# Kernel optimization log

Measured on AMD Instinct MI355X. Metric: run time of the kernel, lower is better.

## Reference

```python
import jax, jax.numpy as jnp
import numpy as np

H = 4       # N_head
C = 32      # c_hidden
CZ = 128    # c_z
N = 256
B = 1
EPS = 1e-5


def setup_inputs() -> dict:
    key = jax.random.key(0)
    ks = jax.random.split(key, 8)
    hc = H * C
    return {
        "z": jax.random.normal(ks[0], (B, N, N, CZ), dtype=jnp.float32),
        "ln_scale": jnp.ones((CZ,), dtype=jnp.float32),
        "ln_bias": jnp.zeros((CZ,), dtype=jnp.float32),
        "Wq": jax.random.normal(ks[1], (CZ, hc), dtype=jnp.float32) * 0.02,
        "Wk": jax.random.normal(ks[2], (CZ, hc), dtype=jnp.float32) * 0.02,
        "Wv": jax.random.normal(ks[3], (CZ, hc), dtype=jnp.float32) * 0.02,
        "Wb": jax.random.normal(ks[4], (CZ, H), dtype=jnp.float32) * 0.02,
        "Wg": jax.random.normal(ks[5], (CZ, hc), dtype=jnp.float32) * 0.02,
        "Wo": jax.random.normal(ks[6], (hc, CZ), dtype=jnp.float32) * 0.02,
    }


def reference(z, ln_scale, ln_bias, Wq, Wk, Wv, Wb, Wg, Wo):
    b, n = z.shape[0], z.shape[1]
    # LayerNorm over c_z
    mu = jnp.mean(z, axis=-1, keepdims=True)
    var = jnp.mean(jnp.square(z - mu), axis=-1, keepdims=True)
    zn = (z - mu) * jax.lax.rsqrt(var + EPS) * ln_scale + ln_bias
    # projections -> [B, N, N, H, C]
    q = (zn @ Wq).reshape(b, n, n, H, C)
    k = (zn @ Wk).reshape(b, n, n, H, C)
    v = (zn @ Wv).reshape(b, n, n, H, C)
    bias = zn @ Wb                                  # [B, N, N, H]
    g = jax.nn.sigmoid(zn @ Wg).reshape(b, n, n, H, C)
    # attention around starting node i: query at (i,j), keys/values at (i,k)
    scores = jnp.einsum('bijhd,bikhd->bijkh', q, k) * (1.0 / C ** 0.5)
    scores = scores + bias[:, None, :, :, :]        # bias[b, j, k, h]
    a = jax.nn.softmax(scores, axis=-2)             # softmax over k
    o = jnp.einsum('bijkh,bikhd->bijhd', a, v)      # [B, N, N, H, C]
    o = (g * o).reshape(b, n, n, H * C)
    return o @ Wo
```

## Files before the change

kernel.cpp:

```cpp
#include <hip/hip_runtime.h>
#include <math.h>

#define NN 256
#define CZ 128
#define NH 4
#define CH 32
#define HC 128
#define NPIX (NN*NN)
#define L2E   1.4426950408889634f
#define SCALE2 (0.17677669529663687f * 1.4426950408889634f)

typedef __attribute__((ext_vector_type(8))) short bf16x8;
typedef __attribute__((ext_vector_type(4))) float fx4;
typedef __attribute__((ext_vector_type(4))) unsigned u32x4;

__device__ __forceinline__ unsigned pack_hl(float x) {
    unsigned b  = __builtin_bit_cast(unsigned, x);
    unsigned hb = b & 0xFFFF0000u;
    float r = x - __builtin_bit_cast(float, hb);
    return hb | (__builtin_bit_cast(unsigned, r) >> 16);
}
__device__ __forceinline__ void load_split8(const float* p, bf16x8& h, bf16x8& l) {
    float4 x0 = *(const float4*)p;
    float4 x1 = *(const float4*)(p + 4);
    float xs[8] = {x0.x, x0.y, x0.z, x0.w, x1.x, x1.y, x1.z, x1.w};
    #pragma unroll
    for (int j = 0; j < 8; ++j) {
        unsigned b  = __builtin_bit_cast(unsigned, xs[j]);
        unsigned hb = b & 0xFFFF0000u;
        float r = xs[j] - __builtin_bit_cast(float, hb);
        h[j] = (short)(hb >> 16);
        l[j] = (short)(__builtin_bit_cast(unsigned, r) >> 16);
    }
}
__device__ __forceinline__ void deint8(const unsigned* p, bf16x8& h, bf16x8& l) {
    u32x4 e0 = *(const u32x4*)p;
    u32x4 e1 = *(const u32x4*)(p + 4);
    unsigned es[8] = {e0[0], e0[1], e0[2], e0[3], e1[0], e1[1], e1[2], e1[3]};
    unsigned hw[4], lw[4];
    #pragma unroll
    for (int j = 0; j < 4; ++j) {
        unsigned a = es[2 * j], b = es[2 * j + 1];
        hw[j] = (a >> 16) | (b & 0xFFFF0000u);
        lw[j] = (a & 0x0000FFFFu) | (b << 16);
    }
    h = __builtin_bit_cast(bf16x8, u32x4{hw[0], hw[1], hw[2], hw[3]});
    l = __builtin_bit_cast(bf16x8, u32x4{lw[0], lw[1], lw[2], lw[3]});
}

__device__ __forceinline__ void qtrans(unsigned &x, unsigned &y) {
#if __has_builtin(__builtin_amdgcn_permlane32_swap) && __has_builtin(__builtin_amdgcn_permlane16_swap)
    {
        auto r = __builtin_amdgcn_permlane32_swap(x, y, false, false);
        x = r[0]; y = r[1];
    }
    {
        auto r = __builtin_amdgcn_permlane16_swap(x, y, false, false);
        x = r[0]; y = r[1];
    }
#else
    asm("v_permlane32_swap_b32 %0, %1\n\t"
        "v_permlane16_swap_b32 %0, %1" : "+v"(x), "+v"(y));
#endif
}

__global__ __launch_bounds__(256) void pack_w_kernel(
    const float* __restrict__ Wq, const float* __restrict__ Wk,
    const float* __restrict__ Wv, const float* __restrict__ Wg,
    const float* __restrict__ Wo, bf16x8* __restrict__ pk)
{
    int id  = blockIdx.x * 256 + threadIdx.x;
    int mid = id >> 11;
    int e   = id & 2047;
    const float* W = (mid == 0) ? Wq : (mid == 1) ? Wk : (mid == 2) ? Wv : (mid == 3) ? Wg : Wo;
    int quad = e & 3, n = (e >> 2) & 127, ks = e >> 9;
    int k0 = ks * 32 + quad * 8;
    bf16x8 h, l;
    #pragma unroll
    for (int j = 0; j < 8; ++j) {
        float x = W[(size_t)(k0 + j) * 128 + n];
        unsigned b  = __builtin_bit_cast(unsigned, x);
        unsigned hb = b & 0xFFFF0000u;
        float r = x - __builtin_bit_cast(float, hb);
        h[j] = (short)(hb >> 16);
        l[j] = (short)(__builtin_bit_cast(unsigned, r) >> 16);
    }
    pk[(size_t)mid * 4096 + e]        = h;
    pk[(size_t)mid * 4096 + 2048 + e] = l;
}

__global__ __launch_bounds__(256) void ln_proj_kernel(
    const float* __restrict__ z, const float* __restrict__ ls, const float* __restrict__ lb,
    const float* __restrict__ Wb, const bf16x8* __restrict__ pk,
    unsigned* __restrict__ q_pk, unsigned* __restrict__ k_pk, unsigned* __restrict__ v_pk,
    float* __restrict__ g_ws, float* __restrict__ bias_n)
{
    __shared__ float zsh[32][132];
    __shared__ float rsum[256], rsq[256];
    __shared__ float pmu[32], prs[32];

    const int t  = threadIdx.x;
    const int p0 = blockIdx.x * 32;
    const int i  = p0 >> 8;
    const int j0 = p0 & 255;

    const float4* z4 = (const float4*)(z + (size_t)p0 * CZ);
    #pragma unroll
    for (int r = 0; r < 4; ++r) {
        int idx4 = t + 256 * r;
        int p = idx4 >> 5, pos = idx4 & 31;
        *(float4*)&zsh[p][pos * 4] = z4[idx4];
    }
    __syncthreads();

    {
        int p = t >> 3, sg = t & 7;
        float s = 0.f, q = 0.f;
        #pragma unroll
        for (int u = 0; u < 16; ++u) { float x = zsh[p][sg * 16 + u]; s += x; q += x * x; }
        rsum[t] = s; rsq[t] = q;
    }
    __syncthreads();
    if (t < 32) {
        float s = 0.f, q = 0.f;
        #pragma unroll
        for (int g = 0; g < 8; ++g) { s += rsum[t * 8 + g]; q += rsq[t * 8 + g]; }
        float mu  = s * (1.0f / 128.0f);
        float var = q * (1.0f / 128.0f) - mu * mu;
        float a   = var + 1e-5f;
        float r   = rsqrtf(a);
        r = r * (1.5f - 0.5f * a * r * r);
        pmu[t] = mu; prs[t] = r;
    }
    __syncthreads();

    #pragma unroll
    for (int r4 = 0; r4 < 4; ++r4) {
        int idx4 = t + 256 * r4;
        int p = idx4 >> 5, pos = idx4 & 31;
        float4 v  = *(float4*)&zsh[p][pos * 4];
        float4 s4 = ((const float4*)ls)[pos];
        float4 b4 = ((const float4*)lb)[pos];
        float mu = pmu[p], rs = prs[p];
        v.x = (v.x - mu) * rs * s4.x + b4.x;
        v.y = (v.y - mu) * rs * s4.y + b4.y;
        v.z = (v.z - mu) * rs * s4.z + b4.z;
        v.w = (v.w - mu) * rs * s4.w + b4.w;
        *(float4*)&zsh[p][pos * 4] = v;
    }
    __syncthreads();

    const int wv = t >> 6, lane = t & 63;
    const int lrow = lane & 15, quad = lane >> 4;
    const bf16x8* ph = pk + (size_t)wv * 4096;
    const bf16x8* pl = ph + 2048;

    fx4 acc[2][8];
    #pragma unroll
    for (int mr = 0; mr < 2; ++mr)
        #pragma unroll
        for (int nc = 0; nc < 8; ++nc)
            acc[mr][nc] = fx4{0.f, 0.f, 0.f, 0.f};

    #pragma unroll
    for (int ks = 0; ks < 4; ++ks) {
        bf16x8 ah[2], al[2];
        #pragma unroll
        for (int mr = 0; mr < 2; ++mr)
            load_split8(&zsh[mr * 16 + lrow][ks * 32 + quad * 8], ah[mr], al[mr]);
        #pragma unroll
        for (int nc = 0; nc < 8; ++nc) {
            int bi = (ks * 128 + nc * 16 + lrow) * 4 + quad;
            bf16x8 bh = ph[bi], bl = pl[bi];
            #pragma unroll
            for (int mr = 0; mr < 2; ++mr) {
                acc[mr][nc] = __builtin_amdgcn_mfma_f32_16x16x32_bf16(ah[mr], bl, acc[mr][nc], 0, 0, 0);
                acc[mr][nc] = __builtin_amdgcn_mfma_f32_16x16x32_bf16(al[mr], bh, acc[mr][nc], 0, 0, 0);
                acc[mr][nc] = __builtin_amdgcn_mfma_f32_16x16x32_bf16(ah[mr], bh, acc[mr][nc], 0, 0, 0);
            }
        }
    }

    #pragma unroll
    for (int mr = 0; mr < 2; ++mr) {
        #pragma unroll
        for (int nc = 0; nc < 8; ++nc) {
            int cg = nc * 16 + lrow;
            int h = cg >> 5, cc = cg & 31;
            int jl = mr * 16 + quad * 4;
            fx4 a = acc[mr][nc];
            if (wv == 0) {
                unsigned* qp = q_pk + ((size_t)(i * NH + h) * NN + j0 + jl) * CH + cc;
                #pragma unroll
                for (int r = 0; r < 4; ++r) qp[r * CH] = pack_hl(a[r]);
            } else if (wv == 1) {
                unsigned* kp = k_pk + ((size_t)(i * NH + h) * NN + j0 + jl) * CH + cc;
                #pragma unroll
                for (int r = 0; r < 4; ++r) kp[r * CH] = pack_hl(a[r]);
            } else if (wv == 2) {
                u32x4 e = {pack_hl(a[0]), pack_hl(a[1]), pack_hl(a[2]), pack_hl(a[3])};
                *(u32x4*)(v_pk + ((size_t)(i * NH + h) * CH + cc) * NN + j0 + jl) = e;
            } else {
                float* gp = g_ws + (size_t)(p0 + jl) * HC + cg;
                #pragma unroll
                for (int r = 0; r < 4; ++r) gp[r * HC] = 1.0f / (1.0f + __expf(-a[r]));
            }
        }
    }

    if (t < 128) {
        int hh = t >> 5, p = t & 31;
        float b = 0.f;
        for (int d = 0; d < 128; ++d) b = fmaf(zsh[p][d], Wb[d * 4 + hh], b);
        bias_n[(size_t)hh * NPIX + (size_t)i * NN + j0 + p] = b * L2E;
    }
}

__global__ __launch_bounds__(256) void attn_kernel(
    const unsigned* __restrict__ q_pk, const unsigned* __restrict__ k_pk,
    const unsigned* __restrict__ v_pk, const float* __restrict__ g_ws,
    const float* __restrict__ bias_n, float* __restrict__ go_ws)
{
    const int t = threadIdx.x;
    const int wv = t >> 6, lane = t & 63;
    const int lrow = lane & 15, quad = lane >> 4;
    const int h = blockIdx.x & 3, i = blockIdx.x >> 2;
    const int qb = wv * 64;

    const unsigned* qs = q_pk + (size_t)(i * NH + h) * NN * CH;
    const unsigned* ks = k_pk + (size_t)(i * NH + h) * NN * CH;
    const unsigned* vs = v_pk + (size_t)(i * NH + h) * CH * NN;
    const float*    bs = bias_n + (size_t)h * NPIX;

    bf16x8 qh[4], ql[4];
    #pragma unroll
    for (int nt = 0; nt < 4; ++nt)
        deint8(qs + (size_t)(qb + nt * 16 + lrow) * CH + quad * 8, qh[nt], ql[nt]);

    fx4 oacc[2][4];
    #pragma unroll
    for (int ct = 0; ct < 2; ++ct)
        #pragma unroll
        for (int nt = 0; nt < 4; ++nt)
            oacc[ct][nt] = fx4{0.f, 0.f, 0.f, 0.f};
    float lsum[4] = {0.f, 0.f, 0.f, 0.f};

    for (int kb = 0; kb < NN; kb += 32) {
        bf16x8 kh[2], kl_[2];
        #pragma unroll
        for (int mt = 0; mt < 2; ++mt)
            deint8(ks + (size_t)(kb + mt * 16 + lrow) * CH + quad * 8, kh[mt], kl_[mt]);
        bf16x8 vh[2], vl[2];
        #pragma unroll
        for (int ct = 0; ct < 2; ++ct)
            deint8(vs + (size_t)(ct * 16 + lrow) * NN + kb + quad * 8, vh[ct], vl[ct]);

        #pragma unroll
        for (int nt = 0; nt < 4; ++nt) {
            unsigned w0h[2], w1h[2], w0l[2], w1l[2];
            #pragma unroll
            for (int mt = 0; mt < 2; ++mt) {
                float4 bv = *(const float4*)(bs + (size_t)(qb + nt * 16 + lrow) * NN
                                                + kb + mt * 16 + quad * 4);

                fx4 sv = fx4{0.f, 0.f, 0.f, 0.f};
                __builtin_amdgcn_s_setprio(1);
                sv = __builtin_amdgcn_mfma_f32_16x16x32_bf16(kh[mt], ql[nt], sv, 0, 0, 0);
                sv = __builtin_amdgcn_mfma_f32_16x16x32_bf16(kl_[mt], qh[nt], sv, 0, 0, 0);
                sv = __builtin_amdgcn_mfma_f32_16x16x32_bf16(kh[mt], qh[nt], sv, 0, 0, 0);
                __builtin_amdgcn_s_setprio(0);

                float e0 = exp2f(fmaf(sv[0], SCALE2, bv.x));
                float e1 = exp2f(fmaf(sv[1], SCALE2, bv.y));
                float e2 = exp2f(fmaf(sv[2], SCALE2, bv.z));
                float e3 = exp2f(fmaf(sv[3], SCALE2, bv.w));
                lsum[nt] += (e0 + e1) + (e2 + e3);

                unsigned b0 = __builtin_bit_cast(unsigned, e0);
                unsigned b1 = __builtin_bit_cast(unsigned, e1);
                unsigned b2 = __builtin_bit_cast(unsigned, e2);
                unsigned b3 = __builtin_bit_cast(unsigned, e3);
                unsigned h01 = (b0 >> 16) | (b1 & 0xFFFF0000u);
                unsigned h23 = (b2 >> 16) | (b3 & 0xFFFF0000u);
                float r0 = e0 - __builtin_bit_cast(float, b0 & 0xFFFF0000u);
                float r1 = e1 - __builtin_bit_cast(float, b1 & 0xFFFF0000u);
                float r2 = e2 - __builtin_bit_cast(float, b2 & 0xFFFF0000u);
                float r3 = e3 - __builtin_bit_cast(float, b3 & 0xFFFF0000u);
                unsigned l01 = (__builtin_bit_cast(unsigned, r0) >> 16)
                             | (__builtin_bit_cast(unsigned, r1) & 0xFFFF0000u);
                unsigned l23 = (__builtin_bit_cast(unsigned, r2) >> 16)
                             | (__builtin_bit_cast(unsigned, r3) & 0xFFFF0000u);
                w0h[mt] = h01; w1h[mt] = h23;
                w0l[mt] = l01; w1l[mt] = l23;
            }

            qtrans(w0h[0], w0h[1]);
            qtrans(w1h[0], w1h[1]);
            qtrans(w0l[0], w0l[1]);
            qtrans(w1l[0], w1l[1]);
            bf16x8 pbh = __builtin_bit_cast(bf16x8, u32x4{w0h[0], w1h[0], w0h[1], w1h[1]});
            bf16x8 pbl = __builtin_bit_cast(bf16x8, u32x4{w0l[0], w1l[0], w0l[1], w1l[1]});

            __builtin_amdgcn_s_setprio(1);
            #pragma unroll
            for (int ct = 0; ct < 2; ++ct) {
                oacc[ct][nt] = __builtin_amdgcn_mfma_f32_16x16x32_bf16(vh[ct], pbl, oacc[ct][nt], 0, 0, 0);
                oacc[ct][nt] = __builtin_amdgcn_mfma_f32_16x16x32_bf16(vl[ct], pbh, oacc[ct][nt], 0, 0, 0);
                oacc[ct][nt] = __builtin_amdgcn_mfma_f32_16x16x32_bf16(vh[ct], pbh, oacc[ct][nt], 0, 0, 0);
            }
            __builtin_amdgcn_s_setprio(0);
        }
    }

    #pragma unroll
    for (int nt = 0; nt < 4; ++nt) {
        float s = lsum[nt];
        s += __shfl_xor(s, 16, 64);
        s += __shfl_xor(s, 32, 64);
        float inv = 1.0f / s;
        size_t pix = (size_t)i * NN + qb + nt * 16 + lrow;
        #pragma unroll
        for (int ct = 0; ct < 2; ++ct) {
            const float* gp = g_ws + pix * HC + h * CH + ct * 16 + quad * 4;
            float4 g4 = *(const float4*)gp;
            fx4 o = oacc[ct][nt];
            float4 r;
            r.x = g4.x * o[0] * inv;
            r.y = g4.y * o[1] * inv;
            r.z = g4.z * o[2] * inv;
            r.w = g4.w * o[3] * inv;
            *(float4*)(go_ws + pix * HC + h * CH + ct * 16 + quad * 4) = r;
        }
    }
}

__global__ __launch_bounds__(256) void outproj_kernel(
    const float* __restrict__ go_ws, const bf16x8* __restrict__ pk, float* __restrict__ out)
{
    __shared__ float gsh[64][132];
    const int t  = threadIdx.x;
    const int p0 = blockIdx.x * 64;

    const float4* g4 = (const float4*)(go_ws + (size_t)p0 * HC);
    #pragma unroll
    for (int r = 0; r < 8; ++r) {
        int idx4 = t + 256 * r;
        int p = idx4 >> 5, pos = idx4 & 31;
        *(float4*)&gsh[p][pos * 4] = g4[idx4];
    }
    __syncthreads();

    const int wv = t >> 6, lane = t & 63;
    const int lrow = lane & 15, quad = lane >> 4;
    const bf16x8* ph = pk + (size_t)4 * 4096;
    const bf16x8* pl = ph + 2048;

    fx4 acc[8];
    #pragma unroll
    for (int nc = 0; nc < 8; ++nc) acc[nc] = fx4{0.f, 0.f, 0.f, 0.f};

    #pragma unroll
    for (int ks = 0; ks < 4; ++ks) {
        bf16x8 ah, al;
        load_split8(&gsh[wv * 16 + lrow][ks * 32 + quad * 8], ah, al);
        #pragma unroll
        for (int nc = 0; nc < 8; ++nc) {
            int bi = (ks * 128 + nc * 16 + lrow) * 4 + quad;
            bf16x8 bh = ph[bi], bl = pl[bi];
            acc[nc] = __builtin_amdgcn_mfma_f32_16x16x32_bf16(ah, bl, acc[nc], 0, 0, 0);
            acc[nc] = __builtin_amdgcn_mfma_f32_16x16x32_bf16(al, bh, acc[nc], 0, 0, 0);
            acc[nc] = __builtin_amdgcn_mfma_f32_16x16x32_bf16(ah, bh, acc[nc], 0, 0, 0);
        }
    }

    #pragma unroll
    for (int nc = 0; nc < 8; ++nc) {
        #pragma unroll
        for (int r = 0; r < 4; ++r)
            out[(size_t)(p0 + wv * 16 + quad * 4 + r) * HC + nc * 16 + lrow] = acc[nc][r];
    }
}

extern "C" void kernel_launch(void* const* d_in, const int* in_sizes, int n_in,
                              void* d_out, int out_size, void* d_ws, size_t ws_size,
                              hipStream_t stream)
{
    const float* z  = (const float*)d_in[0];
    const float* ls = (const float*)d_in[1];
    const float* lb = (const float*)d_in[2];
    const float* Wq = (const float*)d_in[3];
    const float* Wk = (const float*)d_in[4];
    const float* Wv = (const float*)d_in[5];
    const float* Wb = (const float*)d_in[6];
    const float* Wg = (const float*)d_in[7];
    const float* Wo = (const float*)d_in[8];

    float* ws = (float*)d_ws;
    const size_t BIG = (size_t)NPIX * HC;
    unsigned* q_pk  = (unsigned*)ws;
    unsigned* k_pk  = (unsigned*)(ws + BIG);
    unsigned* v_pk  = (unsigned*)(ws + 2 * BIG);
    float* g_ws     = ws + 3 * BIG;
    float* go_ws    = ws + 4 * BIG;
    float* bias_n   = ws + 5 * BIG;
    bf16x8* pk      = (bf16x8*)(bias_n + (size_t)NH * NPIX);

    pack_w_kernel<<<40, 256, 0, stream>>>(Wq, Wk, Wv, Wg, Wo, pk);
    ln_proj_kernel<<<NPIX / 32, 256, 0, stream>>>(z, ls, lb, Wb, pk,
                                                  q_pk, k_pk, v_pk, g_ws, bias_n);
    attn_kernel<<<NN * NH, 256, 0, stream>>>(q_pk, k_pk, v_pk, g_ws, bias_n, go_ws);
    outproj_kernel<<<NPIX / 64, 256, 0, stream>>>(go_ws, pk, (float*)d_out);
}
```

Baseline: 254.1 us.

## Prefetch next K tile and batch QK MFMAs before softmax in attention loop

The attention loop now issues raw loads for V, bias and the next iteration's K tile at the top, so global latency overlaps with compute (software pipelining of K). It also restructures the inner loop into phases: all QK MFMAs for four query tiles, then all exponentials and packing, then all lane transposes, then all PV MFMAs. Grouping like work this way gives the scheduler longer independent chains. The cost is many more live registers (scores, bias, packed P for all tiles), which may lower occupancy or cause spills.

```diff
diff --git a/kernel.cpp b/kernel.cpp
--- a/kernel.cpp
+++ b/kernel.cpp
@@ -33,9 +33,7 @@
         l[j] = (short)(__builtin_bit_cast(unsigned, r) >> 16);
     }
 }
-__device__ __forceinline__ void deint8(const unsigned* p, bf16x8& h, bf16x8& l) {
-    u32x4 e0 = *(const u32x4*)p;
-    u32x4 e1 = *(const u32x4*)(p + 4);
+__device__ __forceinline__ void deint_raw(u32x4 e0, u32x4 e1, bf16x8& h, bf16x8& l) {
     unsigned es[8] = {e0[0], e0[1], e0[2], e0[3], e1[0], e1[1], e1[2], e1[3]};
     unsigned hw[4], lw[4];
     #pragma unroll
@@ -46,6 +44,11 @@
     }
     h = __builtin_bit_cast(bf16x8, u32x4{hw[0], hw[1], hw[2], hw[3]});
     l = __builtin_bit_cast(bf16x8, u32x4{lw[0], lw[1], lw[2], lw[3]});
+}
+__device__ __forceinline__ void deint8(const unsigned* p, bf16x8& h, bf16x8& l) {
+    u32x4 e0 = *(const u32x4*)p;
+    u32x4 e1 = *(const u32x4*)(p + 4);
+    deint_raw(e0, e1, h, l);
 }
 
 __device__ __forceinline__ void qtrans(unsigned &x, unsigned &y) {
@@ -237,6 +240,13 @@
     for (int nt = 0; nt < 4; ++nt)
         deint8(qs + (size_t)(qb + nt * 16 + lrow) * CH + quad * 8, qh[nt], ql[nt]);
 
+    u32x4 krA[2], krB[2];
+    #pragma unroll
+    for (int mt = 0; mt < 2; ++mt) {
+        const u32x4* kp = (const u32x4*)(ks + (size_t)(mt * 16 + lrow) * CH + quad * 8);
+        krA[mt] = kp[0]; krB[mt] = kp[1];
+    }
+
     fx4 oacc[2][4];
     #pragma unroll
     for (int ct = 0; ct < 2; ++ct)
@@ -246,34 +256,63 @@
     float lsum[4] = {0.f, 0.f, 0.f, 0.f};
 
     for (int kb = 0; kb < NN; kb += 32) {
+        u32x4 vrA[2], vrB[2];
+        #pragma unroll
+        for (int ct = 0; ct < 2; ++ct) {
+            const u32x4* vp = (const u32x4*)(vs + (size_t)(ct * 16 + lrow) * NN + kb + quad * 8);
+            vrA[ct] = vp[0]; vrB[ct] = vp[1];
+        }
+        float4 bv[4][2];
+        #pragma unroll
+        for (int nt = 0; nt < 4; ++nt)
+            #pragma unroll
+            for (int mt = 0; mt < 2; ++mt)
+                bv[nt][mt] = *(const float4*)(bs + (size_t)(qb + nt * 16 + lrow) * NN
+                                                 + kb + mt * 16 + quad * 4);
+        const int kb2 = (kb + 32) & (NN - 1);
+        u32x4 nkA[2], nkB[2];
+        #pragma unroll
+        for (int mt = 0; mt < 2; ++mt) {
+            const u32x4* kp = (const u32x4*)(ks + (size_t)(kb2 + mt * 16 + lrow) * CH + quad * 8);
+            nkA[mt] = kp[0]; nkB[mt] = kp[1];
+        }
+
         bf16x8 kh[2], kl_[2];
         #pragma unroll
         for (int mt = 0; mt < 2; ++mt)
-            deint8(ks + (size_t)(kb + mt * 16 + lrow) * CH + quad * 8, kh[mt], kl_[mt]);
-        bf16x8 vh[2], vl[2];
-        #pragma unroll
-        for (int ct = 0; ct < 2; ++ct)
-            deint8(vs + (size_t)(ct * 16 + lrow) * NN + kb + quad * 8, vh[ct], vl[ct]);
-
+            deint_raw(krA[mt], krB[mt], kh[mt], kl_[mt]);
+
+        fx4 sv[4][2];
+        __builtin_amdgcn_s_setprio(1);
         #pragma unroll
         for (int nt = 0; nt < 4; ++nt) {
-            unsigned w0h[2], w1h[2], w0l[2], w1l[2];
             #pragma unroll
             for (int mt = 0; mt < 2; ++mt) {
-                float4 bv = *(const float4*)(bs + (size_t)(qb + nt * 16 + lrow) * NN
-                                                + kb + mt * 16 + quad * 4);
-
-                fx4 sv = fx4{0.f, 0.f, 0.f, 0.f};
-                __builtin_amdgcn_s_setprio(1);
-                sv = __builtin_amdgcn_mfma_f32_16x16x32_bf16(kh[mt], ql[nt], sv, 0, 0, 0);
-                sv = __builtin_amdgcn_mfma_f32_16x16x32_bf16(kl_[mt], qh[nt], sv, 0, 0, 0);
-                sv = __builtin_amdgcn_mfma_f32_16x16x32_bf16(kh[mt], qh[nt], sv, 0, 0, 0);
-                __builtin_amdgcn_s_setprio(0);
-
-                float e0 = exp2f(fmaf(sv[0], SCALE2, bv.x));
-                float e1 = exp2f(fmaf(sv[1], SCALE2, bv.y));
-                float e2 = exp2f(fmaf(sv[2], SCALE2, bv.z));
-                float e3 = exp2f(fmaf(sv[3], SCALE2, bv.w));
+                fx4 s = fx4{0.f, 0.f, 0.f, 0.f};
+                s = __builtin_amdgcn_mfma_f32_16x16x32_bf16(kh[mt],  ql[nt], s, 0, 0, 0);
+                s = __builtin_amdgcn_mfma_f32_16x16x32_bf16(kl_[mt], qh[nt], s, 0, 0, 0);
+                s = __builtin_amdgcn_mfma_f32_16x16x32_bf16(kh[mt],  qh[nt], s, 0, 0, 0);
+                sv[nt][mt] = s;
+            }
+        }
+        __builtin_amdgcn_s_setprio(0);
+
+        bf16x8 vh[2], vl[2];
+        #pragma unroll
+        for (int ct = 0; ct < 2; ++ct)
+            deint_raw(vrA[ct], vrB[ct], vh[ct], vl[ct]);
+
+        unsigned w0h[4][2], w1h[4][2], w0l[4][2], w1l[4][2];
+        #pragma unroll
+        for (int nt = 0; nt < 4; ++nt) {
+            #pragma unroll
+            for (int mt = 0; mt < 2; ++mt) {
+                fx4 s = sv[nt][mt];
+                float4 b4 = bv[nt][mt];
+                float e0 = exp2f(fmaf(s[0], SCALE2, b4.x));
+                float e1 = exp2f(fmaf(s[1], SCALE2, b4.y));
+                float e2 = exp2f(fmaf(s[2], SCALE2, b4.z));
+                float e3 = exp2f(fmaf(s[3], SCALE2, b4.w));
                 lsum[nt] += (e0 + e1) + (e2 + e3);
 
                 unsigned b0 = __builtin_bit_cast(unsigned, e0);
@@ -290,26 +329,37 @@
                              | (__builtin_bit_cast(unsigned, r1) & 0xFFFF0000u);
                 unsigned l23 = (__builtin_bit_cast(unsigned, r2) >> 16)
                              | (__builtin_bit_cast(unsigned, r3) & 0xFFFF0000u);
-                w0h[mt] = h01; w1h[mt] = h23;
-                w0l[mt] = l01; w1l[mt] = l23;
+                w0h[nt][mt] = h01; w1h[nt][mt] = h23;
+                w0l[nt][mt] = l01; w1l[nt][mt] = l23;
             }
-
-            qtrans(w0h[0], w0h[1]);
-            qtrans(w1h[0], w1h[1]);
-            qtrans(w0l[0], w0l[1]);
-            qtrans(w1l[0], w1l[1]);
-            bf16x8 pbh = __builtin_bit_cast(bf16x8, u32x4{w0h[0], w1h[0], w0h[1], w1h[1]});
-            bf16x8 pbl = __builtin_bit_cast(bf16x8, u32x4{w0l[0], w1l[0], w0l[1], w1l[1]});
-
-            __builtin_amdgcn_s_setprio(1);
+        }
+
+        #pragma unroll
+        for (int nt = 0; nt < 4; ++nt) {
+            qtrans(w0h[nt][0], w0h[nt][1]);
+            qtrans(w1h[nt][0], w1h[nt][1]);
+            qtrans(w0l[nt][0], w0l[nt][1]);
+            qtrans(w1l[nt][0], w1l[nt][1]);
+        }
+
+        __builtin_amdgcn_s_setprio(1);
+        #pragma unroll
+        for (int nt = 0; nt < 4; ++nt) {
+            bf16x8 pbh = __builtin_bit_cast(bf16x8,
+                u32x4{w0h[nt][0], w1h[nt][0], w0h[nt][1], w1h[nt][1]});
+            bf16x8 pbl = __builtin_bit_cast(bf16x8,
+                u32x4{w0l[nt][0], w1l[nt][0], w0l[nt][1], w1l[nt][1]});
             #pragma unroll
             for (int ct = 0; ct < 2; ++ct) {
                 oacc[ct][nt] = __builtin_amdgcn_mfma_f32_16x16x32_bf16(vh[ct], pbl, oacc[ct][nt], 0, 0, 0);
                 oacc[ct][nt] = __builtin_amdgcn_mfma_f32_16x16x32_bf16(vl[ct], pbh, oacc[ct][nt], 0, 0, 0);
                 oacc[ct][nt] = __builtin_amdgcn_mfma_f32_16x16x32_bf16(vh[ct], pbh, oacc[ct][nt], 0, 0, 0);
             }
-            __builtin_amdgcn_s_setprio(0);
-        }
+        }
+        __builtin_amdgcn_s_setprio(0);
+
+        #pragma unroll
+        for (int mt = 0; mt < 2; ++mt) { krA[mt] = nkA[mt]; krB[mt] = nkB[mt]; }
     }
 
     #pragma unroll
```

After: 246.5 us. 1.03x faster.
